# Optimization experiments

Measured on AMD Instinct MI355X. Metric: run time of the kernel, lower is better.

Reference implementation:

```python
import jax, jax.numpy as jnp
import numpy as np

LEVELS = (1, 2, 4)
NHEAD = 4
LN_EPS = 1e-5


def _layernorm(x, g, b):
    m = jnp.mean(x, axis=-1, keepdims=True)
    v = jnp.mean((x - m) ** 2, axis=-1, keepdims=True)
    return (x - m) * jax.lax.rsqrt(v + LN_EPS) * g + b


def _spp_pool(x, starts, ends):
    # Exact AdaptiveAvgPool1d over per-proposal segments via inclusive-prefix-sum.
    # x: [B,C,T]; starts/ends: [B,P] int. Returns [B, P, C*sum(LEVELS)].
    B, C, T = x.shape
    P = starts.shape[1]
    xt = jnp.transpose(x, (0, 2, 1))  # [B,T,C]
    csum = jnp.concatenate([jnp.zeros((B, 1, C), x.dtype), jnp.cumsum(xt, axis=1)], axis=1)  # [B,T+1,C]
    n = ends - starts  # [B,P], always >= 1
    feats = []
    for L in LEVELS:
        i = jnp.arange(L)
        lo = (starts[..., None] + (i * n[..., None]) // L).reshape(B, P * L)
        hi = (starts[..., None] + ((i + 1) * n[..., None] + L - 1) // L).reshape(B, P * L)
        slo = jnp.take_along_axis(csum, lo[..., None], axis=1)  # [B,P*L,C]
        shi = jnp.take_along_axis(csum, hi[..., None], axis=1)
        mean = (shi - slo) / (hi - lo).astype(x.dtype)[..., None]
        # torch view(N, C*L) flattens [C,L] C-major -> transpose bins to last axis
        feats.append(mean.reshape(B, P, L, C).transpose(0, 1, 3, 2).reshape(B, P, C * L))
    return jnp.concatenate(feats, axis=-1)


def _encoder_layer(x, qkv_w, qkv_b, out_w, out_b, g1, b1, w1, bb1, w2, bb2, g2, b2):
    # Post-norm nn.TransformerEncoderLayer with exact-erf gelu, dropout=0 (eval)
    B, P, d = x.shape
    dh = d // NHEAD
    qkv = x @ qkv_w.T + qkv_b  # [B,P,3d]
    q, k, v = jnp.split(qkv, 3, axis=-1)
    sh = lambda t: t.reshape(B, P, NHEAD, dh).transpose(0, 2, 1, 3)  # [B,H,P,dh]
    q, k, v = sh(q), sh(k), sh(v)
    scale = 1.0 / float(np.sqrt(dh))
    attn = jax.nn.softmax(jnp.einsum('bhqd,bhkd->bhqk', q, k) * scale, axis=-1)
    o = jnp.einsum('bhqk,bhkd->bhqd', attn, v).transpose(0, 2, 1, 3).reshape(B, P, d)
    o = o @ out_w.T + out_b
    x = _layernorm(x + o, g1, b1)
    h = jax.nn.gelu(x @ w1.T + bb1, approximate=False) @ w2.T + bb2
    return _layernorm(x + h, g2, b2)


def _forward(x, proposal_boxes, proj_w, proj_b, pos_w1, pos_b1, pos_w2, pos_b2,
             qkv_w, qkv_b, out_w, out_b, ln1_g, ln1_b, ff1_w, ff1_b,
             ff2_w, ff2_b, ln2_g, ln2_b, cls_w, cls_b, det_w, det_b):
    B, C, T = x.shape
    P = proposal_boxes.shape[1]
    starts = jnp.clip(proposal_boxes[..., 0], 0, T - 1)
    ends = jnp.clip(proposal_boxes[..., 1], 1, T)
    ends = jnp.where(ends <= starts, jnp.minimum(starts + 1, T), ends)
    feats = _spp_pool(x, starts, ends)  # [B,P,spp_out_dim]
    s_f = proposal_boxes[..., 0].astype(x.dtype)
    e_f = proposal_boxes[..., 1].astype(x.dtype)
    centers = (s_f + e_f) / 2.0
    lengths = jnp.maximum(e_f - s_f, 1.0)
    pos_feat = jnp.stack([centers / T, lengths / T], axis=-1)  # [B,P,2]
    sort_idx = jnp.argsort(centers, axis=1)
    feats_s = jnp.take_along_axis(feats, sort_idx[..., None], axis=1)
    pos_emb = jax.nn.relu(pos_feat @ pos_w1.T + pos_b1) @ pos_w2.T + pos_b2
    pos_emb_s = jnp.take_along_axis(pos_emb, sort_idx[..., None], axis=1)
    tok = feats_s @ proj_w.T + proj_b + pos_emb_s  # [B,P,d]
    for l in range(qkv_w.shape[0]):
        tok = _encoder_layer(tok, qkv_w[l], qkv_b[l], out_w[l], out_b[l],
                             ln1_g[l], ln1_b[l], ff1_w[l], ff1_b[l],
                             ff2_w[l], ff2_b[l], ln2_g[l], ln2_b[l])
    inv = jnp.argsort(sort_idx, axis=1)
    ctx = jnp.take_along_axis(tok, inv[..., None], axis=1)  # [B,P,d]
    class_logits = ctx @ cls_w.T + cls_b  # [B,P,nc]
    det_logits = ctx @ det_w.T + det_b
    class_prob = jax.nn.softmax(class_logits, axis=2)
    det_prob = jax.nn.softmax(det_logits, axis=1)
    joint_prob = class_prob * det_prob
    video_prob = joint_prob.sum(axis=1)
    return video_prob, joint_prob, class_logits, det_logits, ctx


def setup_inputs() -> dict:
    key = jax.random.key(0)
    ks = jax.random.split(key, 32)
    B, C, T, P = 8, 512, 2048, 512
    d, dff, nc, nl = 512, 1024, 30, 2
    spp_out = C * sum(LEVELS)
    s = 0.02
    f32 = jnp.float32
    inp = {
        'x': jax.random.normal(ks[0], (B, C, T), f32),
        'proposal_boxes': jax.random.randint(ks[1], (B, P, 2), 0, T).astype(jnp.int32),
        'proj_w': jax.random.normal(ks[2], (d, spp_out), f32) * s,
        'proj_b': jnp.zeros((d,), f32),
        'pos_w1': jax.random.normal(ks[3], (d, 2), f32) * s,
        'pos_b1': jnp.zeros((d,), f32),
        'pos_w2': jax.random.normal(ks[4], (d, d), f32) * s,
        'pos_b2': jnp.zeros((d,), f32),
        'qkv_w': jax.random.normal(ks[5], (nl, 3 * d, d), f32) * s,
        'qkv_b': jnp.zeros((nl, 3 * d), f32),
        'out_w': jax.random.normal(ks[6], (nl, d, d), f32) * s,
        'out_b': jnp.zeros((nl, d), f32),
        'ln1_g': jnp.ones((nl, d), f32),
        'ln1_b': jnp.zeros((nl, d), f32),
        'ff1_w': jax.random.normal(ks[7], (nl, dff, d), f32) * s,
        'ff1_b': jnp.zeros((nl, dff), f32),
        'ff2_w': jax.random.normal(ks[8], (nl, d, dff), f32) * s,
        'ff2_b': jnp.zeros((nl, d), f32),
        'ln2_g': jnp.ones((nl, d), f32),
        'ln2_b': jnp.zeros((nl, d), f32),
        'cls_w': jax.random.normal(ks[9], (nc, d), f32) * s,
        'cls_b': jnp.zeros((nc,), f32),
        'det_w': jax.random.normal(ks[10], (nc, d), f32) * s,
        'det_b': jnp.zeros((nc,), f32),
    }
    return inp


def reference(x, proposal_boxes, proj_w, proj_b, pos_w1, pos_b1, pos_w2, pos_b2,
              qkv_w, qkv_b, out_w, out_b, ln1_g, ln1_b, ff1_w, ff1_b,
              ff2_w, ff2_b, ln2_g, ln2_b, cls_w, cls_b, det_w, det_b):
    return _forward(x, proposal_boxes, proj_w, proj_b, pos_w1, pos_b1, pos_w2, pos_b2,
                    qkv_w, qkv_b, out_w, out_b, ln1_g, ln1_b, ff1_w, ff1_b,
                    ff2_w, ff2_b, ln2_g, ln2_b, cls_w, cls_b, det_w, det_b)
```

## Files before the change

kernel.cpp:

```cpp
#include <hip/hip_runtime.h>

#define TDIM 2048
#define CDIM 512
#define BDIM 8
#define PDIM 512
#define DMODEL 512
#define NCOUT 30
#define SPPOUT 3584
#define AKDIM 4096

typedef __attribute__((ext_vector_type(8))) short short8;
typedef __attribute__((ext_vector_type(4))) float f32x4;

typedef const __attribute__((address_space(1))) void* as1cv;
typedef __attribute__((address_space(3))) void* as3v;

__device__ __forceinline__ void gl_lds16(const short* g, short* l){
  __builtin_amdgcn_global_load_lds((as1cv)g, (as3v)l, 16, 0, 0);
}

__device__ __forceinline__ short f2b(float f){
  unsigned u = __float_as_uint(f);
  unsigned r = (u + 0x7fffu + ((u >> 16) & 1u)) >> 16;
  return (short)r;
}

__device__ __forceinline__ float waveSum(float v){
#pragma unroll
  for (int o = 32; o > 0; o >>= 1) v += __shfl_xor(v, o);
  return v;
}
__device__ __forceinline__ float waveMax(float v){
#pragma unroll
  for (int o = 32; o > 0; o >>= 1) v = fmaxf(v, __shfl_xor(v, o));
  return v;
}

__global__ void kzero(float* p, int n){
  int i = blockIdx.x * 256 + threadIdx.x;
  if (i < n) p[i] = 0.f;
}

__global__ void kprep(const float* __restrict__ q, const float* __restrict__ o,
                      const float* __restrict__ f1, const float* __restrict__ f2,
                      const float* __restrict__ cl, const float* __restrict__ dt,
                      short* __restrict__ d){
  int i = blockIdx.x * 256 + threadIdx.x;
  float v;
  if (i < 1572864) v = q[i];
  else if (i < 2097152) v = o[i - 1572864];
  else if (i < 3145728) v = f1[i - 2097152];
  else if (i < 4194304) v = f2[i - 3145728];
  else if (i < 4209664) v = cl[i - 4194304];
  else v = dt[i - 4209664];
  d[i] = f2b(v);
}

__global__ void kscan(const float* __restrict__ x, float* __restrict__ W, float* __restrict__ tot){
  int idx = blockIdx.x;
  int b = idx >> 5, rem = idx & 31, ch = rem >> 1, cg = rem & 1;
  int c = cg * 256 + threadIdx.x;
  const float* xp = x + ((size_t)(b * CDIM + c)) * TDIM + ch * 128;
  float* wp = W + ((size_t)b * TDIM + ch * 128) * CDIM + c;
  float run = 0.f;
  for (int tl = 0; tl < 128; tl += 4){
    float4 v = *(const float4*)(xp + tl);
    run += v.x; wp[(size_t)(tl + 0) * CDIM] = run;
    run += v.y; wp[(size_t)(tl + 1) * CDIM] = run;
    run += v.z; wp[(size_t)(tl + 2) * CDIM] = run;
    run += v.w; wp[(size_t)(tl + 3) * CDIM] = run;
  }
  tot[((size_t)b * 16 + ch) * CDIM + c] = run;
}

__global__ void koff(const float* __restrict__ tot, float* __restrict__ off){
  int b = blockIdx.x >> 1, cg = blockIdx.x & 1;
  int c = cg * 256 + threadIdx.x;
  float run = 0.f;
  for (int ch = 0; ch < 16; ++ch){
    off[((size_t)b * 16 + ch) * CDIM + c] = run;
    run += tot[((size_t)b * 16 + ch) * CDIM + c];
  }
}

__global__ void ksort(const int* __restrict__ boxes, int* __restrict__ sidx){
  __shared__ unsigned key[PDIM];
  int b = blockIdx.x, t = threadIdx.x;
  int s = boxes[(size_t)(b * PDIM + t) * 2];
  int e = boxes[(size_t)(b * PDIM + t) * 2 + 1];
  key[t] = ((unsigned)(s + e) << 9) | (unsigned)t;
  __syncthreads();
  for (int k = 2; k <= PDIM; k <<= 1){
    for (int j = k >> 1; j > 0; j >>= 1){
      int ixj = t ^ j;
      if (ixj > t){
        unsigned a = key[t], c2 = key[ixj];
        bool up = ((t & k) == 0);
        bool doswap = up ? (a > c2) : (a < c2);
        if (doswap){ key[t] = c2; key[ixj] = a; }
      }
      __syncthreads();
    }
  }
  sidx[b * PDIM + t] = (int)(key[t] & 511u);
}

__global__ void kwcat(const float* __restrict__ pw, const float* __restrict__ pw2, short* __restrict__ Wc){
  int i = blockIdx.x * 256 + threadIdx.x;
  int r = i >> 12, k = i & 4095;
  float v = (k < SPPOUT) ? pw[(size_t)r * SPPOUT + k] : pw2[(size_t)r * DMODEL + (k - SPPOUT)];
  Wc[i] = f2b(v);
}

__global__ void kbcat(const float* __restrict__ pb, const float* __restrict__ pb2,
                      const float* __restrict__ cb, const float* __restrict__ db,
                      float* __restrict__ bc, float* __restrict__ bh){
  int i = blockIdx.x * 256 + threadIdx.x;
  if (i < DMODEL) bc[i] = pb[i] + pb2[i];
  if (blockIdx.x == 0 && i < 60) bh[i] = (i < 30) ? cb[i] : db[i - 30];
}

__global__ void kspp(const float* __restrict__ W, const float* __restrict__ off,
                     const int* __restrict__ boxes, const int* __restrict__ sidx,
                     const float* __restrict__ pw1, const float* __restrict__ pb1,
                     short* __restrict__ A){
  int blk = blockIdx.x;
  int b = blk >> 9, j = blk & 511;
  int p = sidx[b * PDIM + j];
  int s0 = boxes[(size_t)(b * PDIM + p) * 2];
  int e0 = boxes[(size_t)(b * PDIM + p) * 2 + 1];
  int start = min(max(s0, 0), TDIM - 1);
  int end   = min(max(e0, 1), TDIM);
  if (end <= start) end = min(start + 1, TDIM);
  int n = end - start;

  int lo[7], hi[7], cb[7], cl[7];
  {
    const int Ls[3] = {1, 2, 4};
    const int Bo[3] = {0, 512, 1536};
    int q = 0;
    for (int li = 0; li < 3; ++li){
      int L = Ls[li];
      for (int i = 0; i < L; ++i){
        lo[q] = start + (i * n) / L;
        hi[q] = start + ((i + 1) * n + L - 1) / L;
        cb[q] = Bo[li] + i;
        cl[q] = L;
        ++q;
      }
    }
  }
  float s_f = (float)s0, e_f = (float)e0;
  float px = (s_f + e_f) * 0.5f / (float)TDIM;
  float py = fmaxf(e_f - s_f, 1.f) / (float)TDIM;
  short* Ar = A + (size_t)(b * PDIM + j) * AKDIM;
  const float* Wb = W + (size_t)b * TDIM * CDIM;
  const float* ob = off + (size_t)b * 16 * CDIM;
  for (int c = threadIdx.x; c < CDIM; c += 256){
#pragma unroll
    for (int q = 0; q < 7; ++q){
      int l = lo[q], h = hi[q];
      float fl = (l == 0) ? 0.f : (Wb[(size_t)(l - 1) * CDIM + c] + ob[((l - 1) >> 7) * CDIM + c]);
      float fh = Wb[(size_t)(h - 1) * CDIM + c] + ob[((h - 1) >> 7) * CDIM + c];
      Ar[cb[q] + c * cl[q]] = f2b((fh - fl) / (float)(h - l));
    }
    float hv = pw1[c * 2] * px + pw1[c * 2 + 1] * py + pb1[c];
    Ar[SPPOUT + c] = f2b(fmaxf(hv, 0.f));
  }
}

template<int BN>
__global__ __launch_bounds__(256) void gemm_bt(
    int M, int N, int K,
    const short* __restrict__ A, int lda, long long sAb, long long sAh,
    const short* __restrict__ B, int ldb, long long sBb, long long sBh,
    float* __restrict__ Cf, short* __restrict__ Cb, int ldc, long long sCb, long long sCh,
    int hdiv, float alpha,
    const float* __restrict__ bias, const float* __restrict__ resid, int act)
{
  constexpr int JF = BN / 32;
  __shared__ short As[128 * 64];
  __shared__ short Bs[BN * 64];
  int z = blockIdx.z;
  int zb = z / hdiv, zh = z - zb * hdiv;
  A += (size_t)zb * sAb + (size_t)zh * sAh;
  B += (size_t)zb * sBb + (size_t)zh * sBh;
  size_t coff = (size_t)zb * sCb + (size_t)zh * sCh;
  int rowBase = blockIdx.y * 128, colBase = blockIdx.x * BN;
  int t = threadIdx.x;
  int lane = t & 63;
  int wave = t >> 6;
  int wm = (wave >> 1) * 64, wn = (wave & 1) * (BN / 2);
  int lm = lane & 15, quad = lane >> 4;
  int srow = t >> 3;
  int skw = ((t & 7) * 8) ^ ((srow & 7) * 8);

  const short* Agp[4];
#pragma unroll
  for (int it = 0; it < 4; ++it)
    Agp[it] = A + (size_t)min(rowBase + srow + it * 32, M - 1) * lda + skw;
  const short* Bgp[JF];
#pragma unroll
  for (int it = 0; it < JF; ++it)
    Bgp[it] = B + (size_t)min(colBase + srow + it * 32, N - 1) * ldb + skw;

  f32x4 zero4 = {0.f, 0.f, 0.f, 0.f};
  f32x4 acc[4][JF];
#pragma unroll
  for (int i = 0; i < 4; ++i)
#pragma unroll
    for (int j = 0; j < JF; ++j) acc[i][j] = zero4;

  int axr = (lm & 7) * 8;
  for (int k0 = 0; k0 < K; k0 += 64){
#pragma unroll
    for (int it = 0; it < 4; ++it) gl_lds16(Agp[it] + k0, As + it * 2048 + t * 8);
#pragma unroll
    for (int it = 0; it < JF; ++it) gl_lds16(Bgp[it] + k0, Bs + it * 2048 + t * 8);
    __syncthreads();
#pragma unroll
    for (int h = 0; h < 2; ++h){
      int koff = (h * 32 + quad * 8) ^ axr;
      short8 af[4], bfr[JF];
#pragma unroll
      for (int i = 0; i < 4; ++i)
        af[i] = *(const short8*)(As + (wm + i * 16 + lm) * 64 + koff);
#pragma unroll
      for (int j = 0; j < JF; ++j)
        bfr[j] = *(const short8*)(Bs + (wn + j * 16 + lm) * 64 + koff);
#pragma unroll
      for (int i = 0; i < 4; ++i)
#pragma unroll
        for (int j = 0; j < JF; ++j)
          acc[i][j] = __builtin_amdgcn_mfma_f32_16x16x32_bf16(af[i], bfr[j], acc[i][j], 0, 0, 0);
    }
    __syncthreads();
  }

#pragma unroll
  for (int i = 0; i < 4; ++i){
#pragma unroll
    for (int j = 0; j < JF; ++j){
#pragma unroll
      for (int r = 0; r < 4; ++r){
        int row = rowBase + wm + i * 16 + quad * 4 + r;
        int col = colBase + wn + j * 16 + lm;
        if (row < M && col < N){
          float v = acc[i][j][r] * alpha;
          if (bias) v += bias[col];
          size_t ci = coff + (size_t)row * ldc + col;
          if (resid) v += resid[ci];
          if (act) v = 0.5f * v * (1.f + erff(v * 0.7071067811865476f));
          if (Cf) Cf[ci] = v;
          if (Cb) Cb[ci] = f2b(v);
        }
      }
    }
  }
}

__global__ void kredG1(const float* __restrict__ part, const float* __restrict__ bias,
                       float* __restrict__ tok, short* __restrict__ tokb){
  int i = blockIdx.x * 256 + threadIdx.x;
  float v = part[i] + part[i + 2097152] + part[i + 4194304] + part[i + 6291456] + bias[i & 511];
  tok[i] = v;
  tokb[i] = f2b(v);
}

__global__ void ksm_rows(const float* __restrict__ S, short* __restrict__ Sb){
  int row = blockIdx.x, lane = threadIdx.x;
  const float* p = S + (size_t)row * 512;
  short* q = Sb + (size_t)row * 512;
  float v[8]; float m = -1e30f;
#pragma unroll
  for (int i = 0; i < 8; ++i){ v[i] = p[lane + 64 * i]; m = fmaxf(m, v[i]); }
  m = waveMax(m);
  float s = 0.f;
#pragma unroll
  for (int i = 0; i < 8; ++i){ v[i] = expf(v[i] - m); s += v[i]; }
  s = waveSum(s);
  float r = 1.f / s;
#pragma unroll
  for (int i = 0; i < 8; ++i) q[lane + 64 * i] = f2b(v[i] * r);
}

__global__ void kvt(const short* __restrict__ qkvb, short* __restrict__ Vt){
  __shared__ short T[32][33];
  int bh = blockIdx.x, pt = blockIdx.y, nt = blockIdx.z;
  int b = bh >> 2, h = bh & 3;
  int tx = threadIdx.x, ty = threadIdx.y;
  const short* src = qkvb + (size_t)(b * 512) * 1536 + 1024 + h * 128;
  int p0 = pt * 32, n0 = nt * 32;
#pragma unroll
  for (int q = 0; q < 4; ++q)
    T[ty * 4 + q][tx] = src[(size_t)(p0 + ty * 4 + q) * 1536 + n0 + tx];
  __syncthreads();
  short* dst = Vt + (size_t)bh * 128 * 512;
#pragma unroll
  for (int q = 0; q < 4; ++q)
    dst[(size_t)(n0 + ty * 4 + q) * 512 + p0 + tx] = T[tx][ty * 4 + q];
}

__global__ void kln(const float* __restrict__ X, float* __restrict__ Y, short* __restrict__ Yb,
                    const float* __restrict__ g, const float* __restrict__ bb){
  int row = blockIdx.x, lane = threadIdx.x;
  const float* xr = X + (size_t)row * DMODEL;
  float v[8]; float s = 0.f;
#pragma unroll
  for (int i = 0; i < 8; ++i){ v[i] = xr[lane + 64 * i]; s += v[i]; }
  s = waveSum(s);
  float m = s * (1.f / DMODEL);
  float q = 0.f;
#pragma unroll
  for (int i = 0; i < 8; ++i){ float d = v[i] - m; q += d * d; }
  q = waveSum(q);
  float inv = rsqrtf(q * (1.f / DMODEL) + 1e-5f);
  float* yr = Y + (size_t)row * DMODEL;
  short* yb = Yb + (size_t)row * DMODEL;
#pragma unroll
  for (int i = 0; i < 8; ++i){
    int c = lane + 64 * i;
    float o = (v[i] - m) * inv * g[c] + bb[c];
    yr[c] = o;
    yb[c] = f2b(o);
  }
}

__global__ void kdetsm(const float* __restrict__ hd, float* __restrict__ dp){
  int b = blockIdx.x / NCOUT, c = blockIdx.x % NCOUT, lane = threadIdx.x;
  float v[8]; float m = -1e30f;
#pragma unroll
  for (int i = 0; i < 8; ++i){
    v[i] = hd[((size_t)(b * PDIM) + lane + 64 * i) * 60 + 30 + c];
    m = fmaxf(m, v[i]);
  }
  m = waveMax(m);
  float s = 0.f;
#pragma unroll
  for (int i = 0; i < 8; ++i){ v[i] = expf(v[i] - m); s += v[i]; }
  s = waveSum(s);
  float r = 1.f / s;
#pragma unroll
  for (int i = 0; i < 8; ++i)
    dp[((size_t)(b * PDIM) + lane + 64 * i) * NCOUT + c] = v[i] * r;
}

__global__ void kfinal(const float* __restrict__ hd, const float* __restrict__ dps,
                       const float* __restrict__ tok, const int* __restrict__ sidx,
                       float* __restrict__ out){
  int blk = blockIdx.x;
  int b = blk >> 9, j = blk & 511;
  int lane = threadIdx.x;
  int p = sidx[b * PDIM + j];
  float* video = out;
  float* joint = out + 240;
  float* clso  = out + 123120;
  float* deto  = out + 246000;
  float* ctxo  = out + 368880;
  size_t rs60 = (size_t)(b * PDIM + j) * 60;
  size_t rs30 = (size_t)(b * PDIM + j) * NCOUT;
  size_t ro = (size_t)(b * PDIM + p) * NCOUT;
  float lc = (lane < NCOUT) ? hd[rs60 + lane] : -1e30f;
  float m = waveMax(lc);
  float e = (lane < NCOUT) ? expf(lc - m) : 0.f;
  float s = waveSum(e);
  float cp = e / s;
  if (lane < NCOUT){
    float dv  = hd[rs60 + 30 + lane];
    float dpv = dps[rs30 + lane];
    float jp  = cp * dpv;
    clso[ro + lane] = lc;
    deto[ro + lane] = dv;
    joint[ro + lane] = jp;
    atomicAdd(&video[b * NCOUT + lane], jp);
  }
  const float* tr = tok + (size_t)(b * PDIM + j) * DMODEL;
  float* cr = ctxo + (size_t)(b * PDIM + p) * DMODEL;
  for (int c = lane; c < DMODEL; c += 64) cr[c] = tr[c];
}

extern "C" void kernel_launch(void* const* d_in, const int* in_sizes, int n_in,
                              void* d_out, int out_size, void* d_ws, size_t ws_size,
                              hipStream_t stream) {
  const float* x      = (const float*)d_in[0];
  const int*   boxes  = (const int*)d_in[1];
  const float* proj_w = (const float*)d_in[2];
  const float* proj_b = (const float*)d_in[3];
  const float* pos_w1 = (const float*)d_in[4];
  const float* pos_b1 = (const float*)d_in[5];
  const float* pos_w2 = (const float*)d_in[6];
  const float* pos_b2 = (const float*)d_in[7];
  const float* qkv_w  = (const float*)d_in[8];
  const float* qkv_b  = (const float*)d_in[9];
  const float* out_w  = (const float*)d_in[10];
  const float* out_b  = (const float*)d_in[11];
  const float* ln1_g  = (const float*)d_in[12];
  const float* ln1_b  = (const float*)d_in[13];
  const float* ff1_w  = (const float*)d_in[14];
  const float* ff1_b  = (const float*)d_in[15];
  const float* ff2_w  = (const float*)d_in[16];
  const float* ff2_b  = (const float*)d_in[17];
  const float* ln2_g  = (const float*)d_in[18];
  const float* ln2_b  = (const float*)d_in[19];
  const float* cls_w  = (const float*)d_in[20];
  const float* cls_b  = (const float*)d_in[21];
  const float* det_w  = (const float*)d_in[22];
  const float* det_b  = (const float*)d_in[23];
  float* out = (float*)d_out;
  float* ws  = (float*)d_ws;

  const size_t oR1    = 0;
  const size_t oS     = 9437184;
  const size_t oSbf   = 17825792;
  const size_t oTok   = 22020096;
  const size_t oTokb  = 24117248;
  const size_t oTok2  = 25165824;
  const size_t oTok2b = 27262976;
  const size_t oWcat  = 28311552;
  const size_t oBcat  = 29360128;
  const size_t oWq    = 29360640;
  const size_t oWo    = 30147072;
  const size_t oWf1   = 30409216;
  const size_t oWf2   = 30933504;
  const size_t oWcls  = 31457792;
  const size_t oWdet  = 31465472;
  const size_t oTot   = 31473152;
  const size_t oOff   = 31538688;
  const size_t oSidx  = 31604224;
  const size_t oBhead = oTot;

  short* Abf   = (short*)(ws + oR1);
  short* qkvb  = (short*)(ws + oR1);
  short* Vt    = (short*)(ws + oR1 + 3145728);
  short* obufb = (short*)(ws + oR1 + 4194304);
  float* x1    = ws + oR1 + 5242880;
  short* hbufb = (short*)(ws + oR1 + 7340032);
  float* headS = ws + oR1 + 5242880;
  float* dpS   = ws + oR1 + 5488640;
  float* csum  = ws + oS;
  float* Cpart = ws + oS;
  float* S     = ws + oS;
  short* Sbf   = (short*)(ws + oSbf);
  float* tok   = ws + oTok;
  short* tokb  = (short*)(ws + oTokb);
  float* tok2  = ws + oTok2;
  short* tok2b = (short*)(ws + oTok2b);
  short* Wcatb = (short*)(ws + oWcat);
  float* bcat  = ws + oBcat;
  short* Wq    = (short*)(ws + oWq);
  short* Wo    = (short*)(ws + oWo);
  short* Wf1   = (short*)(ws + oWf1);
  short* Wf2   = (short*)(ws + oWf2);
  short* Whead = (short*)(ws + oWcls);
  float* tot   = ws + oTot;
  float* offp  = ws + oOff;
  int*   sidx  = (int*)(ws + oSidx);
  float* bhead = ws + oBhead;

  kzero<<<1, 256, 0, stream>>>(out, 240);
  kscan<<<256, 256, 0, stream>>>(x, csum, tot);
  koff<<<16, 256, 0, stream>>>(tot, offp);
  ksort<<<BDIM, 512, 0, stream>>>(boxes, sidx);
  kwcat<<<8192, 256, 0, stream>>>(proj_w, pos_w2, Wcatb);
  kbcat<<<2, 256, 0, stream>>>(proj_b, pos_b2, cls_b, det_b, bcat, bhead);
  kprep<<<16504, 256, 0, stream>>>(qkv_w, out_w, ff1_w, ff2_w, cls_w, det_w, Wq);
  kspp<<<BDIM * PDIM, 256, 0, stream>>>(csum, offp, boxes, sidx, pos_w1, pos_b1, Abf);

  gemm_bt<128><<<dim3(4, 32, 4), 256, 0, stream>>>(
      4096, 512, 1024, Abf, 4096, 1024, 0, Wcatb, 4096, 1024, 0,
      Cpart, nullptr, 512, 2097152, 0, 1, 1.f, nullptr, nullptr, 0);
  kredG1<<<8192, 256, 0, stream>>>(Cpart, bcat, tok, tokb);

  const float scale = 0.08838834764831845f;
  for (int l = 0; l < 2; ++l){
    const short* qw  = Wq  + (size_t)l * 1536 * 512;
    const short* ow  = Wo  + (size_t)l * 512 * 512;
    const short* f1w = Wf1 + (size_t)l * 1024 * 512;
    const short* f2w = Wf2 + (size_t)l * 512 * 1024;
    const float* qb  = qkv_b + (size_t)l * 1536;
    const float* obv = out_b + (size_t)l * 512;
    const float* f1b = ff1_b + (size_t)l * 1024;
    const float* f2b_ = ff2_b + (size_t)l * 512;

    gemm_bt<64><<<dim3(24, 32, 1), 256, 0, stream>>>(
        4096, 1536, 512, tokb, 512, 0, 0, qw, 512, 0, 0,
        nullptr, qkvb, 1536, 0, 0, 1, 1.f, qb, nullptr, 0);
    gemm_bt<128><<<dim3(4, 4, 32), 256, 0, stream>>>(
        512, 512, 128,
        qkvb, 1536, (long long)512 * 1536, 128,
        qkvb + 512, 1536, (long long)512 * 1536, 128,
        S, nullptr, 512, (long long)4 * 512 * 512, (long long)512 * 512,
        4, scale, nullptr, nullptr, 0);
    ksm_rows<<<32 * 512, 64, 0, stream>>>(S, Sbf);
    kvt<<<dim3(32, 16, 4), dim3(32, 8), 0, stream>>>(qkvb, Vt);
    gemm_bt<64><<<dim3(2, 4, 32), 256, 0, stream>>>(
        512, 128, 512,
        Sbf, 512, (long long)4 * 512 * 512, (long long)512 * 512,
        Vt, 512, (long long)4 * 128 * 512, (long long)128 * 512,
        nullptr, obufb, 512, (long long)512 * 512, 128,
        4, 1.f, nullptr, nullptr, 0);
    gemm_bt<64><<<dim3(8, 32, 1), 256, 0, stream>>>(
        4096, 512, 512, obufb, 512, 0, 0, ow, 512, 0, 0,
        x1, nullptr, 512, 0, 0, 1, 1.f, obv, tok, 0);
    kln<<<4096, 64, 0, stream>>>(x1, tok2, tok2b, ln1_g + l * 512, ln1_b + l * 512);
    gemm_bt<64><<<dim3(16, 32, 1), 256, 0, stream>>>(
        4096, 1024, 512, tok2b, 512, 0, 0, f1w, 512, 0, 0,
        nullptr, hbufb, 1024, 0, 0, 1, 1.f, f1b, nullptr, 1);
    gemm_bt<64><<<dim3(8, 32, 1), 256, 0, stream>>>(
        4096, 512, 1024, hbufb, 1024, 0, 0, f2w, 1024, 0, 0,
        x1, nullptr, 512, 0, 0, 1, 1.f, f2b_, tok2, 0);
    kln<<<4096, 64, 0, stream>>>(x1, tok, tokb, ln2_g + l * 512, ln2_b + l * 512);
  }

  gemm_bt<64><<<dim3(1, 32, 1), 256, 0, stream>>>(
      4096, 60, 512, tokb, 512, 0, 0, Whead, 512, 0, 0,
      headS, nullptr, 60, 0, 0, 1, 1.f, bhead, nullptr, 0);
  kdetsm<<<BDIM * NCOUT, 64, 0, stream>>>(headS, dpS);
  kfinal<<<BDIM * PDIM, 64, 0, stream>>>(headS, dpS, tok, sidx, out);
}
```

Before: 567.1 us.

## Split-K small GEMMs, fuse reduction into LayerNorm, merge prep and attention aux kernels

Merges the weight-concat, bias-concat and weight-cast kernels into one launch, and merges the softmax and V-transpose kernels into one launch. The PV, out-projection and FF2 GEMMs are split along K into two partial outputs, which are then reduced by a separate kernel (PV) or inside a fused bias+residual+LayerNorm kernel (out-projection and FF2). The first projection GEMM moves to 64-wide tiles with more blocks. The aim is to fill more CUs on these small GEMMs and cut launch count, at the cost of extra fp32 partial-sum traffic.

Measured after the change: 549.7 us. 1.03x faster.

```diff
diff --git a/kernel.cpp b/kernel.cpp
--- a/kernel.cpp
+++ b/kernel.cpp
@@ -41,19 +41,34 @@
   if (i < n) p[i] = 0.f;
 }
 
-__global__ void kprep(const float* __restrict__ q, const float* __restrict__ o,
-                      const float* __restrict__ f1, const float* __restrict__ f2,
-                      const float* __restrict__ cl, const float* __restrict__ dt,
-                      short* __restrict__ d){
+__global__ void kprep2(const float* __restrict__ pw, const float* __restrict__ pw2,
+                       const float* __restrict__ qw, const float* __restrict__ ow,
+                       const float* __restrict__ f1, const float* __restrict__ f2,
+                       const float* __restrict__ cl, const float* __restrict__ dt,
+                       const float* __restrict__ pb, const float* __restrict__ pb2,
+                       const float* __restrict__ cb, const float* __restrict__ db,
+                       short* __restrict__ Wc, short* __restrict__ Wd,
+                       float* __restrict__ bc, float* __restrict__ bh){
   int i = blockIdx.x * 256 + threadIdx.x;
-  float v;
-  if (i < 1572864) v = q[i];
-  else if (i < 2097152) v = o[i - 1572864];
-  else if (i < 3145728) v = f1[i - 2097152];
-  else if (i < 4194304) v = f2[i - 3145728];
-  else if (i < 4209664) v = cl[i - 4194304];
-  else v = dt[i - 4209664];
-  d[i] = f2b(v);
+  if (i < 2097152){
+    int r = i >> 12, k = i & 4095;
+    float v = (k < SPPOUT) ? pw[(size_t)r * SPPOUT + k] : pw2[(size_t)r * DMODEL + (k - SPPOUT)];
+    Wc[i] = f2b(v);
+  } else if (i < 6322176){
+    int j = i - 2097152;
+    float v;
+    if (j < 1572864) v = qw[j];
+    else if (j < 2097152) v = ow[j - 1572864];
+    else if (j < 3145728) v = f1[j - 2097152];
+    else if (j < 4194304) v = f2[j - 3145728];
+    else if (j < 4209664) v = cl[j - 4194304];
+    else v = dt[j - 4209664];
+    Wd[j] = f2b(v);
+  } else {
+    int k = i - 6322176;
+    if (k < 512) bc[k] = pb[k] + pb2[k];
+    else if (k < 572) bh[k - 512] = (k < 542) ? cb[k - 512] : db[k - 542];
+  }
 }
 
 __global__ void kscan(const float* __restrict__ x, float* __restrict__ W, float* __restrict__ tot){
@@ -103,21 +118,6 @@
     }
   }
   sidx[b * PDIM + t] = (int)(key[t] & 511u);
-}
-
-__global__ void kwcat(const float* __restrict__ pw, const float* __restrict__ pw2, short* __restrict__ Wc){
-  int i = blockIdx.x * 256 + threadIdx.x;
-  int r = i >> 12, k = i & 4095;
-  float v = (k < SPPOUT) ? pw[(size_t)r * SPPOUT + k] : pw2[(size_t)r * DMODEL + (k - SPPOUT)];
-  Wc[i] = f2b(v);
-}
-
-__global__ void kbcat(const float* __restrict__ pb, const float* __restrict__ pb2,
-                      const float* __restrict__ cb, const float* __restrict__ db,
-                      float* __restrict__ bc, float* __restrict__ bh){
-  int i = blockIdx.x * 256 + threadIdx.x;
-  if (i < DMODEL) bc[i] = pb[i] + pb2[i];
-  if (blockIdx.x == 0 && i < 60) bh[i] = (i < 30) ? cb[i] : db[i - 30];
 }
 
 __global__ void kspp(const float* __restrict__ W, const float* __restrict__ off,
@@ -267,47 +267,29 @@
   tokb[i] = f2b(v);
 }
 
-__global__ void ksm_rows(const float* __restrict__ S, short* __restrict__ Sb){
+__global__ void kredPV(const float* __restrict__ part, short* __restrict__ ob){
+  int i = blockIdx.x * 256 + threadIdx.x;
+  int n = i & 127;
+  int h = (i >> 7) & 3;
+  int q = (i >> 9) & 511;
+  int b = i >> 18;
+  int src = (((b << 2) + h) << 16) + (q << 7) + n;
+  ob[i] = f2b(part[src] + part[src + 2097152]);
+}
+
+__global__ void klnR(const float* __restrict__ part, const float* __restrict__ bias,
+                     const float* __restrict__ resid,
+                     const float* __restrict__ g, const float* __restrict__ bb,
+                     float* __restrict__ Yf, short* __restrict__ Yb){
   int row = blockIdx.x, lane = threadIdx.x;
-  const float* p = S + (size_t)row * 512;
-  short* q = Sb + (size_t)row * 512;
-  float v[8]; float m = -1e30f;
-#pragma unroll
-  for (int i = 0; i < 8; ++i){ v[i] = p[lane + 64 * i]; m = fmaxf(m, v[i]); }
-  m = waveMax(m);
-  float s = 0.f;
-#pragma unroll
-  for (int i = 0; i < 8; ++i){ v[i] = expf(v[i] - m); s += v[i]; }
-  s = waveSum(s);
-  float r = 1.f / s;
-#pragma unroll
-  for (int i = 0; i < 8; ++i) q[lane + 64 * i] = f2b(v[i] * r);
-}
-
-__global__ void kvt(const short* __restrict__ qkvb, short* __restrict__ Vt){
-  __shared__ short T[32][33];
-  int bh = blockIdx.x, pt = blockIdx.y, nt = blockIdx.z;
-  int b = bh >> 2, h = bh & 3;
-  int tx = threadIdx.x, ty = threadIdx.y;
-  const short* src = qkvb + (size_t)(b * 512) * 1536 + 1024 + h * 128;
-  int p0 = pt * 32, n0 = nt * 32;
-#pragma unroll
-  for (int q = 0; q < 4; ++q)
-    T[ty * 4 + q][tx] = src[(size_t)(p0 + ty * 4 + q) * 1536 + n0 + tx];
-  __syncthreads();
-  short* dst = Vt + (size_t)bh * 128 * 512;
-#pragma unroll
-  for (int q = 0; q < 4; ++q)
-    dst[(size_t)(n0 + ty * 4 + q) * 512 + p0 + tx] = T[tx][ty * 4 + q];
-}
-
-__global__ void kln(const float* __restrict__ X, float* __restrict__ Y, short* __restrict__ Yb,
-                    const float* __restrict__ g, const float* __restrict__ bb){
-  int row = blockIdx.x, lane = threadIdx.x;
-  const float* xr = X + (size_t)row * DMODEL;
+  size_t base = (size_t)row * DMODEL;
   float v[8]; float s = 0.f;
 #pragma unroll
-  for (int i = 0; i < 8; ++i){ v[i] = xr[lane + 64 * i]; s += v[i]; }
+  for (int i = 0; i < 8; ++i){
+    int c = lane + 64 * i;
+    v[i] = part[base + c] + part[base + c + 2097152] + bias[c] + resid[base + c];
+    s += v[i];
+  }
   s = waveSum(s);
   float m = s * (1.f / DMODEL);
   float q = 0.f;
@@ -315,14 +297,49 @@
   for (int i = 0; i < 8; ++i){ float d = v[i] - m; q += d * d; }
   q = waveSum(q);
   float inv = rsqrtf(q * (1.f / DMODEL) + 1e-5f);
-  float* yr = Y + (size_t)row * DMODEL;
-  short* yb = Yb + (size_t)row * DMODEL;
 #pragma unroll
   for (int i = 0; i < 8; ++i){
     int c = lane + 64 * i;
     float o = (v[i] - m) * inv * g[c] + bb[c];
-    yr[c] = o;
-    yb[c] = f2b(o);
+    Yf[base + c] = o;
+    Yb[base + c] = f2b(o);
+  }
+}
+
+__global__ void kattn(const float* __restrict__ S, short* __restrict__ Sb,
+                      const short* __restrict__ qkvb, short* __restrict__ Vt){
+  __shared__ short T[32][33];
+  int blk = blockIdx.x, t = threadIdx.x;
+  if (blk < 4096){
+    int row = blk * 4 + (t >> 6), lane = t & 63;
+    const float* p = S + (size_t)row * 512;
+    short* q = Sb + (size_t)row * 512;
+    float v[8]; float m = -1e30f;
+#pragma unroll
+    for (int i = 0; i < 8; ++i){ v[i] = p[lane + 64 * i]; m = fmaxf(m, v[i]); }
+    m = waveMax(m);
+    float s = 0.f;
+#pragma unroll
+    for (int i = 0; i < 8; ++i){ v[i] = expf(v[i] - m); s += v[i]; }
+    s = waveSum(s);
+    float r = 1.f / s;
+#pragma unroll
+    for (int i = 0; i < 8; ++i) q[lane + 64 * i] = f2b(v[i] * r);
+  } else {
+    int bid = blk - 4096;
+    int bh = bid >> 6, pt = (bid >> 2) & 15, nt = bid & 3;
+    int b = bh >> 2, h = bh & 3;
+    int tx = t & 31, ty = t >> 5;
+    const short* src = qkvb + (size_t)(b * 512) * 1536 + 1024 + h * 128;
+    int p0 = pt * 32, n0 = nt * 32;
+#pragma unroll
+    for (int q = 0; q < 4; ++q)
+      T[ty * 4 + q][tx] = src[(size_t)(p0 + ty * 4 + q) * 1536 + n0 + tx];
+    __syncthreads();
+    short* dst = Vt + (size_t)bh * 128 * 512;
+#pragma unroll
+    for (int q = 0; q < 4; ++q)
+      dst[(size_t)(n0 + ty * 4 + q) * 512 + p0 + tx] = T[tx][ty * 4 + q];
   }
 }
 
@@ -423,7 +440,6 @@
   const size_t oWf1   = 30409216;
   const size_t oWf2   = 30933504;
   const size_t oWcls  = 31457792;
-  const size_t oWdet  = 31465472;
   const size_t oTot   = 31473152;
   const size_t oOff   = 31538688;
   const size_t oSidx  = 31604224;
@@ -433,13 +449,13 @@
   short* qkvb  = (short*)(ws + oR1);
   short* Vt    = (short*)(ws + oR1 + 3145728);
   short* obufb = (short*)(ws + oR1 + 4194304);
-  float* x1    = ws + oR1 + 5242880;
-  short* hbufb = (short*)(ws + oR1 + 7340032);
-  float* headS = ws + oR1 + 5242880;
-  float* dpS   = ws + oR1 + 5488640;
+  short* hbufb = (short*)(ws + oR1 + 5242880);
+  float* headS = ws + oR1 + 7340032;
+  float* dpS   = ws + oR1 + 7585792;
   float* csum  = ws + oS;
   float* Cpart = ws + oS;
   float* S     = ws + oS;
+  float* Cp2   = ws + oS;
   short* Sbf   = (short*)(ws + oSbf);
   float* tok   = ws + oTok;
   short* tokb  = (short*)(ws + oTokb);
@@ -461,12 +477,11 @@
   kscan<<<256, 256, 0, stream>>>(x, csum, tot);
   koff<<<16, 256, 0, stream>>>(tot, offp);
   ksort<<<BDIM, 512, 0, stream>>>(boxes, sidx);
-  kwcat<<<8192, 256, 0, stream>>>(proj_w, pos_w2, Wcatb);
-  kbcat<<<2, 256, 0, stream>>>(proj_b, pos_b2, cls_b, det_b, bcat, bhead);
-  kprep<<<16504, 256, 0, stream>>>(qkv_w, out_w, ff1_w, ff2_w, cls_w, det_w, Wq);
+  kprep2<<<24699, 256, 0, stream>>>(proj_w, pos_w2, qkv_w, out_w, ff1_w, ff2_w, cls_w, det_w,
+                                    proj_b, pos_b2, cls_b, det_b, Wcatb, Wq, bcat, bhead);
   kspp<<<BDIM * PDIM, 256, 0, stream>>>(csum, offp, boxes, sidx, pos_w1, pos_b1, Abf);
 
-  gemm_bt<128><<<dim3(4, 32, 4), 256, 0, stream>>>(
+  gemm_bt<64><<<dim3(8, 32, 4), 256, 0, stream>>>(
       4096, 512, 1024, Abf, 4096, 1024, 0, Wcatb, 4096, 1024, 0,
       Cpart, nullptr, 512, 2097152, 0, 1, 1.f, nullptr, nullptr, 0);
   kredG1<<<8192, 256, 0, stream>>>(Cpart, bcat, tok, tokb);
@@ -491,25 +506,25 @@
         qkvb + 512, 1536, (long long)512 * 1536, 128,
         S, nullptr, 512, (long long)4 * 512 * 512, (long long)512 * 512,
         4, scale, nullptr, nullptr, 0);
-    ksm_rows<<<32 * 512, 64, 0, stream>>>(S, Sbf);
-    kvt<<<dim3(32, 16, 4), dim3(32, 8), 0, stream>>>(qkvb, Vt);
-    gemm_bt<64><<<dim3(2, 4, 32), 256, 0, stream>>>(
-        512, 128, 512,
-        Sbf, 512, (long long)4 * 512 * 512, (long long)512 * 512,
-        Vt, 512, (long long)4 * 128 * 512, (long long)128 * 512,
-        nullptr, obufb, 512, (long long)512 * 512, 128,
-        4, 1.f, nullptr, nullptr, 0);
-    gemm_bt<64><<<dim3(8, 32, 1), 256, 0, stream>>>(
-        4096, 512, 512, obufb, 512, 0, 0, ow, 512, 0, 0,
-        x1, nullptr, 512, 0, 0, 1, 1.f, obv, tok, 0);
-    kln<<<4096, 64, 0, stream>>>(x1, tok2, tok2b, ln1_g + l * 512, ln1_b + l * 512);
+    kattn<<<6144, 256, 0, stream>>>(S, Sbf, qkvb, Vt);
+    gemm_bt<64><<<dim3(2, 4, 64), 256, 0, stream>>>(
+        512, 128, 256,
+        Sbf, 512, 256, (long long)512 * 512,
+        Vt, 512, 256, (long long)128 * 512,
+        Cp2, nullptr, 128, 2097152, (long long)512 * 128,
+        32, 1.f, nullptr, nullptr, 0);
+    kredPV<<<8192, 256, 0, stream>>>(Cp2, obufb);
+    gemm_bt<64><<<dim3(8, 32, 2), 256, 0, stream>>>(
+        4096, 512, 256, obufb, 512, 256, 0, ow, 512, 256, 0,
+        Cp2, nullptr, 512, 2097152, 0, 1, 1.f, nullptr, nullptr, 0);
+    klnR<<<4096, 64, 0, stream>>>(Cp2, obv, tok, ln1_g + l * 512, ln1_b + l * 512, tok2, tok2b);
     gemm_bt<64><<<dim3(16, 32, 1), 256, 0, stream>>>(
         4096, 1024, 512, tok2b, 512, 0, 0, f1w, 512, 0, 0,
         nullptr, hbufb, 1024, 0, 0, 1, 1.f, f1b, nullptr, 1);
-    gemm_bt<64><<<dim3(8, 32, 1), 256, 0, stream>>>(
-        4096, 512, 1024, hbufb, 1024, 0, 0, f2w, 1024, 0, 0,
-        x1, nullptr, 512, 0, 0, 1, 1.f, f2b_, tok2, 0);
-    kln<<<4096, 64, 0, stream>>>(x1, tok, tokb, ln2_g + l * 512, ln2_b + l * 512);
+    gemm_bt<64><<<dim3(8, 32, 2), 256, 0, stream>>>(
+        4096, 512, 512, hbufb, 1024, 512, 0, f2w, 1024, 512, 0,
+        Cp2, nullptr, 512, 2097152, 0, 1, 1.f, nullptr, nullptr, 0);
+    klnR<<<4096, 64, 0, stream>>>(Cp2, f2b_, tok2, ln2_g + l * 512, ln2_b + l * 512, tok, tokb);
   }
 
   gemm_bt<64><<<dim3(1, 32, 1), 256, 0, stream>>>(
```
